# Optimization experiments

Hardware: AMD Instinct MI355X
Metric: run time of the kernel (lower is better)

## Reference

```python
import jax, jax.numpy as jnp
import numpy as np

ENC_VOCAB = 16000
DEC_VOCAB = 16000
HIDDEN = 1024
EMB = 512
ATTN = 512
MAX_STEPS = 512
NEG_INF = -1e30


def gru_cell(x, h, W_ih, W_hh, b_ih, b_hh):
    # torch GRU cell math. x:[B,I], h:[B,H], W_ih:[3H,I], W_hh:[3H,H]
    gi = x @ W_ih.T + b_ih
    gh = h @ W_hh.T + b_hh
    i_r, i_z, i_n = jnp.split(gi, 3, axis=1)
    h_r, h_z, h_n = jnp.split(gh, 3, axis=1)
    r = jax.nn.sigmoid(i_r + h_r)
    z = jax.nn.sigmoid(i_z + h_z)
    n = jnp.tanh(i_n + r * h_n)
    return (1.0 - z) * n + z * h


def setup_inputs() -> dict:
    key = jax.random.key(0)
    ks = jax.random.split(key, 16)
    B, T = 4, 128
    inputs = jax.random.randint(ks[0], (B, T), 0, ENC_VOCAB)

    def p(k, shape, fan_in):
        return (jax.random.normal(k, shape, dtype=jnp.float32) / np.sqrt(fan_in)).astype(jnp.float32)

    enc_emb = p(ks[1], (ENC_VOCAB, EMB), EMB)
    enc_Wih = p(ks[2], (3 * HIDDEN, EMB), EMB)
    enc_Whh = p(ks[3], (3 * HIDDEN, HIDDEN), HIDDEN)
    enc_bih = jnp.zeros((3 * HIDDEN,), jnp.float32)
    enc_bhh = jnp.zeros((3 * HIDDEN,), jnp.float32)
    dec_emb = p(ks[4], (DEC_VOCAB, EMB), EMB)
    dec_emb = dec_emb.at[0].set(0.0)  # padding_idx=0
    dec_Wih = p(ks[5], (3 * HIDDEN, EMB + ATTN), EMB + ATTN)
    dec_Whh = p(ks[6], (3 * HIDDEN, HIDDEN), HIDDEN)
    dec_bih = jnp.zeros((3 * HIDDEN,), jnp.float32)
    dec_bhh = jnp.zeros((3 * HIDDEN,), jnp.float32)
    W_av = p(ks[7], (ATTN, 2 * HIDDEN), 2 * HIDDEN)
    b_av = jnp.zeros((ATTN,), jnp.float32)
    W_cls = p(ks[8], (DEC_VOCAB, ATTN), ATTN)
    b_cls = jnp.zeros((DEC_VOCAB,), jnp.float32)
    return {
        "inputs": inputs,
        "enc_emb": enc_emb, "enc_Wih": enc_Wih, "enc_Whh": enc_Whh,
        "enc_bih": enc_bih, "enc_bhh": enc_bhh,
        "dec_emb": dec_emb, "dec_Wih": dec_Wih, "dec_Whh": dec_Whh,
        "dec_bih": dec_bih, "dec_bhh": dec_bhh,
        "W_av": W_av, "b_av": b_av, "W_cls": W_cls, "b_cls": b_cls,
    }


def seq2seq_forward(inputs, enc_emb, enc_Wih, enc_Whh, enc_bih, enc_bhh,
                    dec_emb, dec_Wih, dec_Whh, dec_bih, dec_bhh,
                    W_av, b_av, W_cls, b_cls):
    B, T = inputs.shape
    mask = inputs != 0  # [B,T]

    # ---- Encoder GRU (scan over time) ----
    emb = enc_emb[inputs]  # [B,T,E]
    h0 = jnp.zeros((B, HIDDEN), jnp.float32)

    def enc_step(h, x_t):
        h = gru_cell(x_t, h, enc_Wih, enc_Whh, enc_bih, enc_bhh)
        return h, h

    enc_ht, enc_outs = jax.lax.scan(enc_step, h0, jnp.swapaxes(emb, 0, 1))
    enc_outputs = jnp.swapaxes(enc_outs, 0, 1)  # [B,T,H]

    # ---- Decoder: 512 greedy steps ----
    ids0 = jnp.zeros((B,), jnp.int32)
    av0 = jnp.zeros((B, ATTN), jnp.float32)

    def dec_step(carry, _):
        ids, attn_vec, h = carry
        x = jnp.concatenate([dec_emb[ids], attn_vec], axis=1)  # [B,E+A]
        h = gru_cell(x, h, dec_Wih, dec_Whh, dec_bih, dec_bhh)  # [B,H]
        # attention: score = enc_outputs . h
        score = jnp.einsum('bth,bh->bt', enc_outputs, h)
        score = jnp.where(mask, score, NEG_INF)
        w = jax.nn.softmax(score, axis=1)  # [B,T]
        context = jnp.einsum('bt,bth->bh', w, enc_outputs)  # [B,H]
        merged = jnp.concatenate([context, h], axis=1)  # [B,2H]
        attn_vec = jnp.tanh(merged @ W_av.T + b_av)  # [B,A]
        logits = attn_vec @ W_cls.T + b_cls  # [B,V]
        ids = jnp.argmax(logits, axis=1).astype(jnp.int32)
        return (ids, attn_vec, h), (logits, w)

    _, (predictions, attn_weights) = jax.lax.scan(
        dec_step, (ids0, av0, enc_ht), None, length=MAX_STEPS)
    return predictions, attn_weights  # [512,B,V], [512,B,T]


def reference(inputs, enc_emb, enc_Wih, enc_Whh, enc_bih, enc_bhh,
              dec_emb, dec_Wih, dec_Whh, dec_bih, dec_bhh,
              W_av, b_av, W_cls, b_cls):
    return seq2seq_forward(inputs, enc_emb, enc_Wih, enc_Whh, enc_bih, enc_bhh,
                           dec_emb, dec_Wih, dec_Whh, dec_bih, dec_bhh,
                           W_av, b_av, W_cls, b_cls)
```

## Files before the change

kernel.cpp:

```cpp
#include <hip/hip_runtime.h>
#include <stdint.h>

typedef unsigned int u32;
typedef unsigned long long u64;

#define NBLK 256
#define NTHR 1024
#define Bz 4
#define Tz 128
#define Hz 1024
#define Ez 512
#define Az 512
#define Vz 16000
#define NSTEPS 512
#define XS 1032


__device__ __forceinline__ float sigf(float x) { return 1.0f / (1.0f + expf(-x)); }

__device__ __forceinline__ u32 ld_rlx(const u32* p) {
  return __hip_atomic_load(p, __ATOMIC_RELAXED, __HIP_MEMORY_SCOPE_AGENT);
}
__device__ __forceinline__ void st_rel(u32* p, u32 v) {
  __hip_atomic_store(p, v, __ATOMIC_RELEASE, __HIP_MEMORY_SCOPE_AGENT);
}

__device__ __forceinline__ void poll256(const u32* sq, u32 tgt) {
  if (threadIdx.x < 64) {
    const int l = threadIdx.x;
    while (true) {
      u32 m0 = ld_rlx(sq + l);
      u32 m1 = ld_rlx(sq + l + 64);
      u32 m2 = ld_rlx(sq + l + 128);
      u32 m3 = ld_rlx(sq + l + 192);
      u32 a = m0 < m1 ? m0 : m1;
      u32 b = m2 < m3 ? m2 : m3;
      u32 mn = a < b ? a : b;
      if (__all(mn >= tgt)) break;
      __builtin_amdgcn_s_sleep(2);
    }
    if (l == 0)
      (void)__hip_atomic_load(sq, __ATOMIC_ACQUIRE, __HIP_MEMORY_SCOPE_AGENT);
  }
  __syncthreads();
}

__device__ __forceinline__ void poll16(const u32* sq, u32 tgt) {
  if (threadIdx.x < 64) {
    while (true) {
      u32 v = (threadIdx.x < 16) ? ld_rlx(sq + threadIdx.x) : 0xFFFFFFFFu;
      if (__all(v >= tgt)) break;
      __builtin_amdgcn_s_sleep(2);
    }
    if (threadIdx.x == 0)
      (void)__hip_atomic_load(sq, __ATOMIC_ACQUIRE, __HIP_MEMORY_SCOPE_AGENT);
  }
  __syncthreads();
}

template <int K, int L>
__device__ __forceinline__ float idot(const float4* __restrict__ w4,
                                      const float4* __restrict__ v4, int lane) {
  float4 acc = make_float4(0.f, 0.f, 0.f, 0.f);
#pragma unroll 8
  for (int k = 0; k < K; ++k) {
    float4 a = w4[lane + L * k];
    float4 b = v4[lane + L * k];
    acc.x += a.x * b.x; acc.y += a.y * b.y; acc.z += a.z * b.z; acc.w += a.w * b.w;
  }
  return (acc.x + acc.y) + (acc.z + acc.w);
}

__device__ __forceinline__ void bar_arrive(u32* ctrl, int epoch) {
  __syncthreads();
  if (threadIdx.x == 0) {
    const u32 target = (u32)epoch * 16u;
    u32* grp = ctrl + ((blockIdx.x >> 4) * 16);
    u32 v = __hip_atomic_fetch_add(grp, 1u, __ATOMIC_RELEASE, __HIP_MEMORY_SCOPE_AGENT);
    if (v == target - 1u) {
      u32 r = __hip_atomic_fetch_add(ctrl + 256, 1u, __ATOMIC_ACQ_REL, __HIP_MEMORY_SCOPE_AGENT);
      if (r == target - 1u)
        __hip_atomic_store(ctrl + 320, (u32)epoch, __ATOMIC_RELEASE, __HIP_MEMORY_SCOPE_AGENT);
    }
  }
}

__device__ __forceinline__ void bar_wait(u32* ctrl, int epoch) {
  if (threadIdx.x == 0) {
    while (__hip_atomic_load(ctrl + 320, __ATOMIC_RELAXED, __HIP_MEMORY_SCOPE_AGENT) < (u32)epoch)
      __builtin_amdgcn_s_sleep(4);
    (void)__hip_atomic_load(ctrl + 320, __ATOMIC_ACQUIRE, __HIP_MEMORY_SCOPE_AGENT);
  }
  __syncthreads();
}

__global__ void __launch_bounds__(NTHR, 1) seq2seq_kernel(
    const int* __restrict__ inputs,
    const float* __restrict__ enc_emb, const float* __restrict__ enc_Wih,
    const float* __restrict__ enc_Whh, const float* __restrict__ enc_bih,
    const float* __restrict__ enc_bhh,
    const float* __restrict__ dec_emb, const float* __restrict__ dec_Wih,
    const float* __restrict__ dec_Whh, const float* __restrict__ dec_bih,
    const float* __restrict__ dec_bhh,
    const float* __restrict__ W_av, const float* __restrict__ b_av,
    const float* __restrict__ W_cls, const float* __restrict__ b_cls,
    float* __restrict__ out, char* __restrict__ ws) {
  const int tid = threadIdx.x;
  const int bid = blockIdx.x;

  u32* ctrl = (u32*)ws;
  u32* hseq = (u32*)(ws + 8192);
  u32* avseq = (u32*)(ws + 9216);
  u32* amseq = (u32*)(ws + 10240);
  float* h_g = (float*)(ws + 16384);
  float* av_g = (float*)(ws + 49152);
  u64* amax_g = (u64*)(ws + 57344);
  float* encout_g = (float*)(ws + 65536);
  float* pt_g = encout_g + Bz * Tz * Hz;
  float* out_pred = out;
  float* out_aw = out + (long)NSTEPS * Bz * Vz;

  __shared__ __align__(16) float wlds[24][XS];
  __shared__ __align__(16) float x_s[Bz][XS];
  __shared__ __align__(16) float h_s[Bz][XS];
  __shared__ __align__(16) float at_s[Bz][516];
  __shared__ __align__(16) float hb_s[XS];
  __shared__ __align__(16) float e1_s[132];
  __shared__ float sc_s[128];
  __shared__ float qh_s[128];
  __shared__ float g_s[Bz][6][4];
  __shared__ float sinv_s;
  __shared__ int ids_s[Bz];
  __shared__ u64 am_s[Bz][64];

  const int jbase = bid * 4;
  const int t8 = tid >> 3, l8 = tid & 7;
  const int b8 = t8 / 24;
  const int r6 = t8 % 24;
  const int g6 = r6 >> 2, jl = r6 & 3;
  const int lrow = r6;
  const int grow = ((g6 < 3) ? g6 : g6 - 3) * Hz + jbase + jl;

  for (int idx = tid; idx < 12 * Ez; idx += NTHR) {
    int lr = idx >> 9, c = idx & 511;
    wlds[lr][c] = enc_Wih[(long)((lr >> 2) * Hz + jbase + (lr & 3)) * Ez + c];
  }
  for (int idx = tid; idx < 12 * Hz; idx += NTHR) {
    int lr = idx >> 10, c = idx & 1023;
    wlds[12 + lr][c] = enc_Whh[(long)((lr >> 2) * Hz + jbase + (lr & 3)) * Hz + c];
  }
  float gbias = 0.f;
  if (t8 < 96) gbias = (g6 < 3) ? enc_bih[grow] : enc_bhh[grow];
  __syncthreads();

  for (int t = 0; t < Tz; ++t) {
    poll256(hseq, (u32)t);
    float* hrd = h_g + (t & 1) * (Bz * Hz);
    float* hwr = h_g + ((t + 1) & 1) * (Bz * Hz);
    for (int idx = tid; idx < Bz * Ez; idx += NTHR) {
      int b = idx >> 9, k = idx & 511;
      x_s[b][k] = enc_emb[(long)inputs[b * Tz + t] * Ez + k];
    }
    for (int idx = tid; idx < Bz * Hz; idx += NTHR)
      h_s[idx >> 10][idx & 1023] = hrd[idx];
    __syncthreads();
    if (t8 < 96) {
      const float4* w4 = (const float4*)&wlds[lrow][0];
      float acc;
      if (g6 < 3) acc = idot<16, 8>(w4, (const float4*)&x_s[b8][0], l8);
      else        acc = idot<32, 8>(w4, (const float4*)&h_s[b8][0], l8);
      acc += __shfl_xor(acc, 1); acc += __shfl_xor(acc, 2); acc += __shfl_xor(acc, 4);
      if (l8 == 0) g_s[b8][g6][jl] = acc + gbias;
    }
    __syncthreads();
    if (tid < 16) {
      int b = tid & 3, jj = tid >> 2;
      int j = jbase + jj;
      float r = sigf(g_s[b][0][jj] + g_s[b][3][jj]);
      float z = sigf(g_s[b][1][jj] + g_s[b][4][jj]);
      float n = tanhf(g_s[b][2][jj] + r * g_s[b][5][jj]);
      float hv = (1.0f - z) * n + z * h_s[b][j];
      hwr[b * Hz + j] = hv;
      encout_g[((long)(b * Tz) + t) * Hz + j] = hv;
    }
    __syncthreads();
    if (tid == 0) st_rel(hseq + bid, (u32)(t + 1));
  }

  poll256(hseq, (u32)Tz);
  {
    int a = (bid >> 2) * 8 + (tid >> 7);
    int bt = (bid & 3) * 128 + (tid & 127);
    int b = bt >> 7, t2 = bt & 127;
    float acc = idot<256, 1>((const float4*)(W_av + (long)a * (2 * Hz)),
                             (const float4*)(encout_g + (long)bt * Hz), 0);
    pt_g[((long)(b * Az) + a) * Tz + t2] = acc;
  }
  bar_arrive(ctrl, 1); bar_wait(ctrl, 1);

  for (int idx = tid; idx < 12 * Hz; idx += NTHR) {
    int lr = idx >> 10, c = idx & 1023;
    long gr = (long)((lr >> 2) * Hz + jbase + (lr & 3));
    wlds[lr][c] = dec_Wih[gr * 1024 + c];
    wlds[12 + lr][c] = dec_Whh[gr * Hz + c];
  }
  if (t8 < 96) gbias = (g6 < 3) ? dec_bih[grow] : dec_bhh[grow];

  const int task16 = tid >> 4, l16 = tid & 15;
  const int nrows = 62 + (bid < 128 ? 1 : 0);
  const int rbase = bid * 62 + (bid < 128 ? bid : 128);
  const int myrow = rbase + (task16 < nrows ? task16 : 0);
  float4 wreg[8];
  {
    const float4* wr4 = (const float4*)(W_cls + (long)myrow * Az);
#pragma unroll
    for (int k = 0; k < 8; ++k) wreg[k] = wr4[l16 + 16 * k];
  }
  const float bclsr = b_cls[myrow];

  const int atn_b = bid & 3;
  const int abase = (bid >> 2) * 128;
  __syncthreads();

  for (int s = 0; s < NSTEPS; ++s) {
    float* hrd = h_g + (s & 1) * (Bz * Hz);
    float* hwr = h_g + ((s & 1) ^ 1) * (Bz * Hz);

    poll256(amseq, (u32)s);
    if (tid < 256) {
      int b = tid >> 6, l = tid & 63;
      u64 best = 0;
#pragma unroll
      for (int g = 0; g < 4; ++g) {
        u64 v = amax_g[(l + 64 * g) * 4 + b];
        best = v > best ? v : best;
      }
      for (int off = 32; off; off >>= 1) {
        u64 o = __shfl_xor(best, off);
        best = o > best ? o : best;
      }
      if (l == 0) ids_s[b] = (int)(0xFFFFFFFFu - (u32)(best & 0xFFFFFFFFull));
    }
    __syncthreads();
    for (int idx = tid; idx < Bz * (Ez + Az); idx += NTHR) {
      int b = idx >> 10, k = idx & 1023;
      x_s[b][k] = (k < Ez) ? dec_emb[(long)ids_s[b] * Ez + k] : av_g[b * Az + (k - Ez)];
    }
    for (int idx = tid; idx < Bz * Hz; idx += NTHR)
      h_s[idx >> 10][idx & 1023] = hrd[idx];
    __syncthreads();
    if (t8 < 96) {
      const float4* w4 = (const float4*)&wlds[lrow][0];
      const float4* v4 = (const float4*)((g6 < 3) ? &x_s[b8][0] : &h_s[b8][0]);
      float acc = idot<32, 8>(w4, v4, l8);
      acc += __shfl_xor(acc, 1); acc += __shfl_xor(acc, 2); acc += __shfl_xor(acc, 4);
      if (l8 == 0) g_s[b8][g6][jl] = acc + gbias;
    }
    __syncthreads();
    if (tid < 16) {
      int b = tid & 3, jj = tid >> 2;
      int j = jbase + jj;
      float r = sigf(g_s[b][0][jj] + g_s[b][3][jj]);
      float z = sigf(g_s[b][1][jj] + g_s[b][4][jj]);
      float n = tanhf(g_s[b][2][jj] + r * g_s[b][5][jj]);
      hwr[b * Hz + j] = (1.0f - z) * n + z * h_s[b][j];
    }
    __syncthreads();
    if (tid == 0) st_rel(hseq + bid, (u32)(Tz + 1 + s));

    if (bid < 16) {
      poll256(hseq, (u32)(Tz + 1 + s));
      const int b = atn_b;
      for (int idx = tid; idx < Hz; idx += NTHR) hb_s[idx] = hwr[b * Hz + idx];
      __syncthreads();
      {
        const int t = tid >> 3;
        float acc = idot<32, 8>((const float4*)(encout_g + ((long)(b * Tz) + t) * Hz),
                                (const float4*)hb_s, l8);
        acc += __shfl_xor(acc, 1); acc += __shfl_xor(acc, 2); acc += __shfl_xor(acc, 4);
        if (l8 == 0) sc_s[t] = (inputs[b * Tz + t] != 0) ? acc : -1e30f;
        const int a = tid >> 3;
        float qa = idot<32, 8>((const float4*)(W_av + (long)(abase + a) * (2 * Hz) + Hz),
                               (const float4*)hb_s, l8);
        qa += __shfl_xor(qa, 1); qa += __shfl_xor(qa, 2); qa += __shfl_xor(qa, 4);
        if (l8 == 0) qh_s[a] = qa;
      }
      __syncthreads();
      if (tid < 64) {
        float s0 = sc_s[tid], s1 = sc_s[64 + tid];
        float m = fmaxf(s0, s1);
#pragma unroll
        for (int off = 32; off; off >>= 1) m = fmaxf(m, __shfl_xor(m, off));
        float e0 = expf(s0 - m), e1 = expf(s1 - m);
        float sum = e0 + e1;
#pragma unroll
        for (int off = 32; off; off >>= 1) sum += __shfl_xor(sum, off);
        e1_s[tid] = e0; e1_s[64 + tid] = e1;
        if (tid == 0) sinv_s = 1.0f / sum;
      }
      __syncthreads();
      {
        const int a = tid >> 3;
        float ctx = idot<4, 8>((const float4*)(pt_g + ((long)(b * Az) + abase + a) * Tz),
                               (const float4*)e1_s, l8);
        ctx += __shfl_xor(ctx, 1); ctx += __shfl_xor(ctx, 2); ctx += __shfl_xor(ctx, 4);
        if (l8 == 0)
          av_g[b * Az + abase + a] = tanhf(ctx * sinv_s + qh_s[a] + b_av[abase + a]);
      }
      if (bid < 4 && tid < 128)
        out_aw[(long)s * (Bz * Tz) + bid * Tz + tid] = e1_s[tid] * sinv_s;
      __syncthreads();
      if (tid == 0) st_rel(avseq + bid, (u32)(s + 1));
    }

    poll16(avseq, (u32)(s + 1));

    for (int idx = tid; idx < Bz * Az; idx += NTHR)
      at_s[idx >> 9][idx & 511] = av_g[idx];
    __syncthreads();
#pragma unroll
    for (int b = 0; b < 4; ++b) {
      const float4* a4 = (const float4*)&at_s[b][0];
      float acc = 0.f;
#pragma unroll
      for (int k = 0; k < 8; ++k) {
        float4 a = a4[l16 + 16 * k];
        acc += wreg[k].x * a.x + wreg[k].y * a.y + wreg[k].z * a.z + wreg[k].w * a.w;
      }
      acc += __shfl_xor(acc, 1); acc += __shfl_xor(acc, 2);
      acc += __shfl_xor(acc, 4); acc += __shfl_xor(acc, 8);
      if (l16 == 0 && task16 < nrows) {
        acc += bclsr;
        out_pred[((long)s * Bz + b) * Vz + myrow] = acc;
        u32 u = __float_as_uint(acc);
        u = (u & 0x80000000u) ? ~u : (u | 0x80000000u);
        am_s[b][task16] = ((u64)u << 32) | (u64)(0xFFFFFFFFu - (u32)myrow);
      }
    }
    __syncthreads();
    if (tid < 256) {
      int b2 = tid >> 6, l = tid & 63;
      u64 best = (l < nrows) ? am_s[b2][l] : 0ull;
      for (int off = 32; off; off >>= 1) {
        u64 o = __shfl_xor(best, off);
        best = o > best ? o : best;
      }
      if (l == 0) amax_g[bid * 4 + b2] = best;
    }
    __syncthreads();
    if (tid == 0) st_rel(amseq + bid, (u32)(s + 1));
  }
}

extern "C" void kernel_launch(void* const* d_in, const int* in_sizes, int n_in,
                              void* d_out, int out_size, void* d_ws, size_t ws_size,
                              hipStream_t stream) {
  const int* inputs = (const int*)d_in[0];
  const float* enc_emb = (const float*)d_in[1];
  const float* enc_Wih = (const float*)d_in[2];
  const float* enc_Whh = (const float*)d_in[3];
  const float* enc_bih = (const float*)d_in[4];
  const float* enc_bhh = (const float*)d_in[5];
  const float* dec_emb = (const float*)d_in[6];
  const float* dec_Wih = (const float*)d_in[7];
  const float* dec_Whh = (const float*)d_in[8];
  const float* dec_bih = (const float*)d_in[9];
  const float* dec_bhh = (const float*)d_in[10];
  const float* W_av = (const float*)d_in[11];
  const float* b_av = (const float*)d_in[12];
  const float* W_cls = (const float*)d_in[13];
  const float* b_cls = (const float*)d_in[14];

  hipMemsetAsync(d_ws, 0, 57344, stream);
  hipMemsetAsync((char*)d_ws + 57344, 0xFF, 8192, stream);

  seq2seq_kernel<<<dim3(NBLK), dim3(NTHR), 0, stream>>>(
      inputs, enc_emb, enc_Wih, enc_Whh, enc_bih, enc_bhh,
      dec_emb, dec_Wih, dec_Whh, dec_bih, dec_bhh,
      W_av, b_av, W_cls, b_cls,
      (float*)d_out, (char*)d_ws);
}
```

Measured before the change: 20.75 ms.

## Restructure decoder step sync: dedicated argmax reducer, split qh projection, counter barrier

Reworks the cross-block synchronization in the persistent decoder loop. Argmax reduction moves to a single reducer block that publishes ids through one flag line, so the other blocks no longer poll 256 flags. The W_av hidden-state projection moves from the 16 attention blocks to 32 separate blocks. The attention-done signal becomes a single atomic counter, and the encoder steps now use the hierarchical barrier instead of all-block polling. This shortens the per-step critical path but adds an extra serial hop through the reducer block and more handoffs between blocks.

```diff
diff --git a/kernel.cpp b/kernel.cpp
--- a/kernel.cpp
+++ b/kernel.cpp
@@ -45,19 +45,6 @@
   __syncthreads();
 }
 
-__device__ __forceinline__ void poll16(const u32* sq, u32 tgt) {
-  if (threadIdx.x < 64) {
-    while (true) {
-      u32 v = (threadIdx.x < 16) ? ld_rlx(sq + threadIdx.x) : 0xFFFFFFFFu;
-      if (__all(v >= tgt)) break;
-      __builtin_amdgcn_s_sleep(2);
-    }
-    if (threadIdx.x == 0)
-      (void)__hip_atomic_load(sq, __ATOMIC_ACQUIRE, __HIP_MEMORY_SCOPE_AGENT);
-  }
-  __syncthreads();
-}
-
 template <int K, int L>
 __device__ __forceinline__ float idot(const float4* __restrict__ w4,
                                       const float4* __restrict__ v4, int lane) {
@@ -110,12 +97,14 @@
 
   u32* ctrl = (u32*)ws;
   u32* hseq = (u32*)(ws + 8192);
-  u32* avseq = (u32*)(ws + 9216);
-  u32* amseq = (u32*)(ws + 10240);
+  u32* amseq = (u32*)(ws + 9216);
+  u32* qhseq = (u32*)(ws + 10240);
+  u32* idsline = (u32*)(ws + 10752);
   float* h_g = (float*)(ws + 16384);
   float* av_g = (float*)(ws + 49152);
   u64* amax_g = (u64*)(ws + 57344);
-  float* encout_g = (float*)(ws + 65536);
+  float* qh_g = (float*)(ws + 65536);
+  float* encout_g = (float*)(ws + 73728);
   float* pt_g = encout_g + Bz * Tz * Hz;
   float* out_pred = out;
   float* out_aw = out + (long)NSTEPS * Bz * Vz;
@@ -127,12 +116,13 @@
   __shared__ __align__(16) float hb_s[XS];
   __shared__ __align__(16) float e1_s[132];
   __shared__ float sc_s[128];
-  __shared__ float qh_s[128];
   __shared__ float g_s[Bz][6][4];
   __shared__ float sinv_s;
   __shared__ int ids_s[Bz];
+  __shared__ int idsred[Bz];
   __shared__ u64 am_s[Bz][64];
 
+  int epoch = 0;
   const int jbase = bid * 4;
   const int t8 = tid >> 3, l8 = tid & 7;
   const int b8 = t8 / 24;
@@ -154,7 +144,6 @@
   __syncthreads();
 
   for (int t = 0; t < Tz; ++t) {
-    poll256(hseq, (u32)t);
     float* hrd = h_g + (t & 1) * (Bz * Hz);
     float* hwr = h_g + ((t + 1) & 1) * (Bz * Hz);
     for (int idx = tid; idx < Bz * Ez; idx += NTHR) {
@@ -183,11 +172,9 @@
       hwr[b * Hz + j] = hv;
       encout_g[((long)(b * Tz) + t) * Hz + j] = hv;
     }
-    __syncthreads();
-    if (tid == 0) st_rel(hseq + bid, (u32)(t + 1));
-  }
-
-  poll256(hseq, (u32)Tz);
+    ++epoch; bar_arrive(ctrl, epoch); bar_wait(ctrl, epoch);
+  }
+
   {
     int a = (bid >> 2) * 8 + (tid >> 7);
     int bt = (bid & 3) * 128 + (tid & 127);
@@ -195,8 +182,8 @@
     float acc = idot<256, 1>((const float4*)(W_av + (long)a * (2 * Hz)),
                              (const float4*)(encout_g + (long)bt * Hz), 0);
     pt_g[((long)(b * Az) + a) * Tz + t2] = acc;
-  }
-  bar_arrive(ctrl, 1); bar_wait(ctrl, 1);
+    ++epoch; bar_arrive(ctrl, epoch); bar_wait(ctrl, epoch);
+  }
 
   for (int idx = tid; idx < 12 * Hz; idx += NTHR) {
     int lr = idx >> 10, c = idx & 1023;
@@ -218,28 +205,23 @@
   }
   const float bclsr = b_cls[myrow];
 
+  const bool is_atn = bid < 16;
+  const bool is_qh = (bid >= 16) && (bid < 48);
+  const bool is_red = bid == 48;
   const int atn_b = bid & 3;
   const int abase = (bid >> 2) * 128;
+  const int qbase = (bid - 16) * 16;
   __syncthreads();
 
   for (int s = 0; s < NSTEPS; ++s) {
     float* hrd = h_g + (s & 1) * (Bz * Hz);
     float* hwr = h_g + ((s & 1) ^ 1) * (Bz * Hz);
 
-    poll256(amseq, (u32)s);
-    if (tid < 256) {
-      int b = tid >> 6, l = tid & 63;
-      u64 best = 0;
-#pragma unroll
-      for (int g = 0; g < 4; ++g) {
-        u64 v = amax_g[(l + 64 * g) * 4 + b];
-        best = v > best ? v : best;
-      }
-      for (int off = 32; off; off >>= 1) {
-        u64 o = __shfl_xor(best, off);
-        best = o > best ? o : best;
-      }
-      if (l == 0) ids_s[b] = (int)(0xFFFFFFFFu - (u32)(best & 0xFFFFFFFFull));
+    if (tid == 0) {
+      while (ld_rlx(idsline) < (u32)s) __builtin_amdgcn_s_sleep(2);
+      (void)__hip_atomic_load(idsline, __ATOMIC_ACQUIRE, __HIP_MEMORY_SCOPE_AGENT);
+      const int* idp = (const int*)(idsline + 1);
+      ids_s[0] = idp[0]; ids_s[1] = idp[1]; ids_s[2] = idp[2]; ids_s[3] = idp[3];
     }
     __syncthreads();
     for (int idx = tid; idx < Bz * (Ez + Az); idx += NTHR) {
@@ -266,10 +248,28 @@
       hwr[b * Hz + j] = (1.0f - z) * n + z * h_s[b][j];
     }
     __syncthreads();
-    if (tid == 0) st_rel(hseq + bid, (u32)(Tz + 1 + s));
-
-    if (bid < 16) {
-      poll256(hseq, (u32)(Tz + 1 + s));
+    if (tid == 0) st_rel(hseq + bid, (u32)(s + 1));
+
+    if (is_qh) {
+      poll256(hseq, (u32)(s + 1));
+      for (int idx = tid; idx < Bz * Hz; idx += NTHR)
+        x_s[idx >> 10][idx & 1023] = hwr[idx];
+      __syncthreads();
+      {
+        int al = task16 >> 2, b = task16 & 3;
+        int a = qbase + al;
+        float qa = idot<16, 16>((const float4*)(W_av + (long)a * (2 * Hz) + Hz),
+                                (const float4*)&x_s[b][0], l16);
+        qa += __shfl_xor(qa, 1); qa += __shfl_xor(qa, 2);
+        qa += __shfl_xor(qa, 4); qa += __shfl_xor(qa, 8);
+        if (l16 == 0) qh_g[b * Az + a] = qa;
+      }
+      __syncthreads();
+      if (tid == 0) st_rel(qhseq + (bid - 16) * 4, (u32)(s + 1));
+    }
+
+    if (is_atn) {
+      poll256(hseq, (u32)(s + 1));
       const int b = atn_b;
       for (int idx = tid; idx < Hz; idx += NTHR) hb_s[idx] = hwr[b * Hz + idx];
       __syncthreads();
@@ -279,11 +279,6 @@
                                 (const float4*)hb_s, l8);
         acc += __shfl_xor(acc, 1); acc += __shfl_xor(acc, 2); acc += __shfl_xor(acc, 4);
         if (l8 == 0) sc_s[t] = (inputs[b * Tz + t] != 0) ? acc : -1e30f;
-        const int a = tid >> 3;
-        float qa = idot<32, 8>((const float4*)(W_av + (long)(abase + a) * (2 * Hz) + Hz),
-                               (const float4*)hb_s, l8);
-        qa += __shfl_xor(qa, 1); qa += __shfl_xor(qa, 2); qa += __shfl_xor(qa, 4);
-        if (l8 == 0) qh_s[a] = qa;
       }
       __syncthreads();
       if (tid < 64) {
@@ -297,6 +292,17 @@
         for (int off = 32; off; off >>= 1) sum += __shfl_xor(sum, off);
         e1_s[tid] = e0; e1_s[64 + tid] = e1;
         if (tid == 0) sinv_s = 1.0f / sum;
+      }
+      __syncthreads();
+      if (tid < 64) {
+        const int sb = (bid >> 2) * 8;
+        while (true) {
+          u32 v = (tid < 8) ? ld_rlx(qhseq + (sb + tid) * 4) : 0xFFFFFFFFu;
+          if (__all(v >= (u32)(s + 1))) break;
+          __builtin_amdgcn_s_sleep(2);
+        }
+        if (tid == 0)
+          (void)__hip_atomic_load(qhseq, __ATOMIC_ACQUIRE, __HIP_MEMORY_SCOPE_AGENT);
       }
       __syncthreads();
       {
@@ -305,15 +311,23 @@
                                (const float4*)e1_s, l8);
         ctx += __shfl_xor(ctx, 1); ctx += __shfl_xor(ctx, 2); ctx += __shfl_xor(ctx, 4);
         if (l8 == 0)
-          av_g[b * Az + abase + a] = tanhf(ctx * sinv_s + qh_s[a] + b_av[abase + a]);
+          av_g[b * Az + abase + a] =
+              tanhf(ctx * sinv_s + qh_g[b * Az + abase + a] + b_av[abase + a]);
       }
       if (bid < 4 && tid < 128)
         out_aw[(long)s * (Bz * Tz) + bid * Tz + tid] = e1_s[tid] * sinv_s;
       __syncthreads();
-      if (tid == 0) st_rel(avseq + bid, (u32)(s + 1));
-    }
-
-    poll16(avseq, (u32)(s + 1));
+      if (tid == 0)
+        __hip_atomic_fetch_add(ctrl + 384, 1u, __ATOMIC_RELEASE, __HIP_MEMORY_SCOPE_AGENT);
+    }
+
+    if (tid == 0) {
+      const u32 tgt = (u32)(16 * (s + 1));
+      while (__hip_atomic_load(ctrl + 384, __ATOMIC_RELAXED, __HIP_MEMORY_SCOPE_AGENT) < tgt)
+        __builtin_amdgcn_s_sleep(8);
+      (void)__hip_atomic_load(ctrl + 384, __ATOMIC_ACQUIRE, __HIP_MEMORY_SCOPE_AGENT);
+    }
+    __syncthreads();
 
     for (int idx = tid; idx < Bz * Az; idx += NTHR)
       at_s[idx >> 9][idx & 511] = av_g[idx];
@@ -349,6 +363,30 @@
     }
     __syncthreads();
     if (tid == 0) st_rel(amseq + bid, (u32)(s + 1));
+
+    if (is_red) {
+      poll256(amseq, (u32)(s + 1));
+      if (tid < 256) {
+        int b = tid >> 6, l = tid & 63;
+        u64 best = 0;
+#pragma unroll
+        for (int g = 0; g < 4; ++g) {
+          u64 v = amax_g[(l + 64 * g) * 4 + b];
+          best = v > best ? v : best;
+        }
+        for (int off = 32; off; off >>= 1) {
+          u64 o = __shfl_xor(best, off);
+          best = o > best ? o : best;
+        }
+        if (l == 0) idsred[b] = (int)(0xFFFFFFFFu - (u32)(best & 0xFFFFFFFFull));
+      }
+      __syncthreads();
+      if (tid == 0) {
+        int* idp = (int*)(idsline + 1);
+        idp[0] = idsred[0]; idp[1] = idsred[1]; idp[2] = idsred[2]; idp[3] = idsred[3];
+        st_rel(idsline, (u32)(s + 1));
+      }
+    }
   }
 }
 
@@ -371,8 +409,7 @@
   const float* W_cls = (const float*)d_in[13];
   const float* b_cls = (const float*)d_in[14];
 
-  hipMemsetAsync(d_ws, 0, 57344, stream);
-  hipMemsetAsync((char*)d_ws + 57344, 0xFF, 8192, stream);
+  hipMemsetAsync(d_ws, 0, 73728, stream);
 
   seq2seq_kernel<<<dim3(NBLK), dim3(NTHR), 0, stream>>>(
       inputs, enc_emb, enc_Wih, enc_Whh, enc_bih, enc_bhh,
```

Result: faster. 18.64 ms (-10.2%).
